# Kernel optimization log

Hardware: AMD Instinct MI355X
Metric: run time of the kernel (lower is better)

Reference implementation:

```python
import jax, jax.numpy as jnp
import numpy as np

CAPS = 16          # num_capsules
DIM = 16           # capsule_dim
NUM_ROUTING = 3
L2_EPS = 1e-12     # tf.nn.l2_normalize epsilon


def setup_inputs() -> dict:
    key = jax.random.key(0)
    k1, k2 = jax.random.split(key)
    inputs = jax.random.normal(k1, (16, 64, 64, 128), dtype=jnp.float32)
    # Conv2D kernel, HWIO layout, fan-in scaled like glorot-ish init
    kernel = jax.random.normal(k2, (3, 3, 128, CAPS * DIM), dtype=jnp.float32) * 0.03
    bias = jnp.zeros((CAPS * DIM,), dtype=jnp.float32)
    return {"inputs": inputs, "kernel": kernel, "bias": bias}


def reference(inputs, kernel, bias):
    # Conv2D(caps*dim, 3x3, padding='same', activation='relu'), channels_last
    x = jax.lax.conv_general_dilated(
        inputs, kernel, window_strides=(1, 1), padding="SAME",
        dimension_numbers=("NHWC", "HWIO", "NHWC"))
    x = jax.nn.relu(x + bias)
    B, H, W, _ = x.shape
    x = x.reshape(B, H * W, CAPS, DIM)            # (B, N, C, D)
    b = jnp.zeros((B, H * W, CAPS), dtype=x.dtype)
    v = None
    for _ in range(NUM_ROUTING):
        c = jax.nn.softmax(b, axis=-1)             # over capsules
        s = jnp.einsum("bnc,bncd->bcd", c, x)      # weighted sum over spatial
        # tf.nn.l2_normalize along last axis
        v = s * jax.lax.rsqrt(jnp.maximum(jnp.sum(s * s, axis=-1, keepdims=True), L2_EPS))
        b = b + jnp.einsum("bncd,bcd->bnc", x, v)  # agreement update
    # tile v over spatial dims: (B,1,1,C*D) -> (B,H,W,C*D)
    out = jnp.broadcast_to(v.reshape(B, 1, 1, CAPS * DIM), (B, H, W, CAPS * DIM))
    return out
```

## Files before the change

### kernel.cpp

```cpp
#include <hip/hip_runtime.h>
#include <hip/hip_bf16.h>

typedef unsigned short u16;
typedef unsigned int   u32;

typedef __bf16 bf16x8 __attribute__((ext_vector_type(8)));
typedef float  f32x4  __attribute__((ext_vector_type(4)));

__device__ __forceinline__ u16 f2b(float f) {
    __hip_bfloat16 h = __float2bfloat16(f);
    u16 u; __builtin_memcpy(&u, &h, 2); return u;
}
__device__ __forceinline__ float blo(u32 u) { return __uint_as_float(u << 16); }
__device__ __forceinline__ float bhi(u32 u) { return __uint_as_float(u & 0xffff0000u); }

__global__ void k_prep(const float* __restrict__ wk,
                       u16* __restrict__ BF, float* __restrict__ stats) {
    int bx = blockIdx.x, tid = threadIdx.x;
    if (bx < 1152) {
        int t = bx * 256 + tid;
        int j  = t & 7;
        int n  = (t >> 3) & 255;
        int q  = (t >> 11) & 3;
        int kk = (t >> 13) & 3;
        int p  = t >> 15;
        BF[t] = f2b(wk[(p * 128 + kk * 32 + q * 8 + j) * 256 + n]);
    } else {
        stats[(bx - 1152) * 256 + tid] = 0.f;
    }
}

__launch_bounds__(512, 4)
__global__ void k_conv(const float* __restrict__ in, const u16* __restrict__ BF,
                       const float* __restrict__ bias,
                       u16* __restrict__ X, float* __restrict__ s0) {
    __shared__ u16 ldsA[25344];
    const int t = threadIdx.x;
    const int lane = t & 63, wid = t >> 6;
    const int q = lane >> 4, l15 = lane & 15;
    const int wr = wid >> 2;
    const int wc = wid & 3;
    const int bb = blockIdx.x >> 6;
    const int h  = blockIdx.x & 63;
    const int wn0 = wc << 6;

#define STAGE_ALL() { \
    float4 fa[7], fb[7]; float zf[7]; \
    _Pragma("unroll") for (int i = 0; i < 7; ++i) { \
        int slot = i * 512 + t; \
        int ok = (i < 6) | (t < 96); \
        int pr = slot / 1056; int rem = slot - pr * 1056; \
        int wp = rem >> 4, cs = rem & 15; \
        int gc = cs ^ (wp & 7); \
        int y = h + pr - 1, x = wp - 1; \
        int inb = ok & ((((unsigned)y < 64u) & ((unsigned)x < 64u)) ? 1 : 0); \
        int ys = inb ? y : 0, xs = inb ? x : 0; \
        const float4* s4 = (const float4*)(in + \
            (((bb * 64 + ys) * 64 + xs) * 128 + gc * 8)); \
        fa[i] = s4[0]; fb[i] = s4[1]; \
        zf[i] = inb ? 1.f : 0.f; \
    } \
    _Pragma("unroll") for (int i = 0; i < 7; ++i) { \
        if (i < 6 || t < 96) { \
            int slot = i * 512 + t; \
            u16 ov[8]; \
            ov[0]=f2b(fa[i].x*zf[i]); ov[1]=f2b(fa[i].y*zf[i]); \
            ov[2]=f2b(fa[i].z*zf[i]); ov[3]=f2b(fa[i].w*zf[i]); \
            ov[4]=f2b(fb[i].x*zf[i]); ov[5]=f2b(fb[i].y*zf[i]); \
            ov[6]=f2b(fb[i].z*zf[i]); ov[7]=f2b(fb[i].w*zf[i]); \
            uint4 wv; __builtin_memcpy(&wv, ov, 16); \
            *(uint4*)((char*)ldsA + slot * 16) = wv; \
        } \
    } }

#define LOADB4(B, P, G) { \
    _Pragma("unroll") for (int ni = 0; ni < 4; ++ni) \
        B[ni] = *(const bf16x8*)(BFl + (P) * 32768 + (G) * 8192 + ni * 128); }

#define COMP4(B, DH, DW, G) { \
    bf16x8 af[2]; \
    _Pragma("unroll") for (int mi = 0; mi < 2; ++mi) { \
        int wp = wr * 32 + mi * 16 + l15 + (DW); \
        int swz = ((G) * 4 + q) ^ (wp & 7); \
        af[mi] = *(const bf16x8*)((const char*)ldsA + \
            (((DH) * 1056 + wp * 16 + swz) << 4)); \
    } \
    _Pragma("unroll") for (int mi = 0; mi < 2; ++mi) \
    _Pragma("unroll") for (int ni = 0; ni < 4; ++ni) \
        acc[mi][ni] = __builtin_amdgcn_mfma_f32_16x16x32_bf16( \
            af[mi], B[ni], acc[mi][ni], 0, 0, 0); }

#define CHAIN() { \
    LOADB4(B0, 0, 2); COMP4(B1, 0, 0, 1); \
    LOADB4(B1, 0, 3); COMP4(B0, 0, 0, 2); \
    LOADB4(B0, 1, 0); COMP4(B1, 0, 0, 3); \
    LOADB4(B1, 1, 1); COMP4(B0, 0, 1, 0); \
    LOADB4(B0, 1, 2); COMP4(B1, 0, 1, 1); \
    LOADB4(B1, 1, 3); COMP4(B0, 0, 1, 2); \
    LOADB4(B0, 2, 0); COMP4(B1, 0, 1, 3); \
    LOADB4(B1, 2, 1); COMP4(B0, 0, 2, 0); \
    LOADB4(B0, 2, 2); COMP4(B1, 0, 2, 1); \
    LOADB4(B1, 2, 3); COMP4(B0, 0, 2, 2); \
    LOADB4(B0, 3, 0); COMP4(B1, 0, 2, 3); \
    LOADB4(B1, 3, 1); COMP4(B0, 1, 0, 0); \
    LOADB4(B0, 3, 2); COMP4(B1, 1, 0, 1); \
    LOADB4(B1, 3, 3); COMP4(B0, 1, 0, 2); \
    LOADB4(B0, 4, 0); COMP4(B1, 1, 0, 3); \
    LOADB4(B1, 4, 1); COMP4(B0, 1, 1, 0); \
    LOADB4(B0, 4, 2); COMP4(B1, 1, 1, 1); \
    LOADB4(B1, 4, 3); COMP4(B0, 1, 1, 2); \
    LOADB4(B0, 5, 0); COMP4(B1, 1, 1, 3); \
    LOADB4(B1, 5, 1); COMP4(B0, 1, 2, 0); \
    LOADB4(B0, 5, 2); COMP4(B1, 1, 2, 1); \
    LOADB4(B1, 5, 3); COMP4(B0, 1, 2, 2); \
    LOADB4(B0, 6, 0); COMP4(B1, 1, 2, 3); \
    LOADB4(B1, 6, 1); COMP4(B0, 2, 0, 0); \
    LOADB4(B0, 6, 2); COMP4(B1, 2, 0, 1); \
    LOADB4(B1, 6, 3); COMP4(B0, 2, 0, 2); \
    LOADB4(B0, 7, 0); COMP4(B1, 2, 0, 3); \
    LOADB4(B1, 7, 1); COMP4(B0, 2, 1, 0); \
    LOADB4(B0, 7, 2); COMP4(B1, 2, 1, 1); \
    LOADB4(B1, 7, 3); COMP4(B0, 2, 1, 2); \
    LOADB4(B0, 8, 0); COMP4(B1, 2, 1, 3); \
    LOADB4(B1, 8, 1); COMP4(B0, 2, 2, 0); \
    LOADB4(B0, 8, 2); COMP4(B1, 2, 2, 1); \
    LOADB4(B1, 8, 3); COMP4(B0, 2, 2, 2); \
                      COMP4(B1, 2, 2, 3); }

    const u16* BFl = BF + (q * 2048 + (wn0 + l15) * 8);

    STAGE_ALL();

    f32x4 zero = {0.f, 0.f, 0.f, 0.f};
    f32x4 acc[2][4];
    #pragma unroll
    for (int mi = 0; mi < 2; ++mi)
        #pragma unroll
        for (int ni = 0; ni < 4; ++ni) acc[mi][ni] = zero;

    bf16x8 B0[4], B1[4];
    LOADB4(B0, 0, 0);
    LOADB4(B1, 0, 1);
    __syncthreads();

    COMP4(B0, 0, 0, 0);
    CHAIN();

    float bv[4];
    #pragma unroll
    for (int ni = 0; ni < 4; ++ni) bv[ni] = bias[wn0 + ni * 16 + l15];
    float colsum[4] = {0.f, 0.f, 0.f, 0.f};
    u16* xrow = X + (((bb << 12) + (h << 6) + wr * 32 + q * 4) * 256) + wn0 + l15;
    #pragma unroll
    for (int mi = 0; mi < 2; ++mi) {
        #pragma unroll
        for (int rr = 0; rr < 4; ++rr) {
            u16* xp = xrow + (mi * 16 + rr) * 256;
            #pragma unroll
            for (int ni = 0; ni < 4; ++ni) {
                float v = acc[mi][ni][rr] + bv[ni];
                v = v > 0.f ? v : 0.f;
                xp[ni * 16] = f2b(v);
                colsum[ni] += v;
            }
        }
    }
    #pragma unroll
    for (int ni = 0; ni < 4; ++ni) {
        float c = colsum[ni];
        c += __shfl_xor(c, 16);
        c += __shfl_xor(c, 32);
        if (lane < 16) atomicAdd(&s0[bb * 256 + wn0 + ni * 16 + l15], c);
    }
#undef STAGE_ALL
#undef LOADB4
#undef COMP4
#undef CHAIN
}

__launch_bounds__(256, 4)
__global__ void k_pass(const u16* __restrict__ X, const float* __restrict__ Sa,
                       const float* __restrict__ Sb, float* __restrict__ Sout,
                       int use2) {
    __shared__ float vs[272];
    __shared__ float red[4 * 272];
    const int t = threadIdx.x, b = blockIdx.y, chunk = blockIdx.x;
    const int c = t & 15, nl = t >> 4;
    const int lane = t & 63, wid = t >> 6;
    {
        float sa = Sa[b * 256 + t];
        float ss = sa * sa;
        #pragma unroll
        for (int off = 1; off < 16; off <<= 1) ss += __shfl_xor(ss, off);
        ss = ss < 1e-12f ? 1e-12f : ss;
        float vv = sa / sqrtf(ss);
        if (use2) {
            float sb = Sb[b * 256 + t];
            float s2v = sb * sb;
            #pragma unroll
            for (int off = 1; off < 16; off <<= 1) s2v += __shfl_xor(s2v, off);
            s2v = s2v < 1e-12f ? 1e-12f : s2v;
            vv += sb / sqrtf(s2v);
        }
        vs[(t >> 4) * 17 + (t & 15)] = vv;
    }
    const u16* xbase = X + ((b << 12) + chunk * 64 + nl) * 256 + c * 16;
    uint4 pa[8];
    #pragma unroll
    for (int r = 0; r < 4; ++r) {
        pa[2 * r]     = ((const uint4*)(xbase + r * 4096))[0];
        pa[2 * r + 1] = ((const uint4*)(xbase + r * 4096))[1];
    }
    __syncthreads();
    float vr[16];
    #pragma unroll
    for (int d = 0; d < 16; ++d) vr[d] = vs[c * 17 + d];

    float acc[16];
    #pragma unroll
    for (int d = 0; d < 16; ++d) acc[d] = 0.f;

    #pragma unroll
    for (int r = 0; r < 4; ++r) {
        u32 us[8];
        __builtin_memcpy(us, &pa[2 * r], 32);
        float xf[16];
        #pragma unroll
        for (int j = 0; j < 8; ++j) { xf[2*j] = blo(us[j]); xf[2*j+1] = bhi(us[j]); }
        float bvv = 0.f;
        #pragma unroll
        for (int d = 0; d < 16; ++d) bvv += xf[d] * vr[d];
        float e = __expf(bvv);
        float sm = e;
        #pragma unroll
        for (int off = 1; off < 16; off <<= 1) sm += __shfl_xor(sm, off);
        float w = e / sm;
        #pragma unroll
        for (int d = 0; d < 16; ++d) acc[d] += w * xf[d];
    }
    #pragma unroll
    for (int d = 0; d < 16; ++d) {
        acc[d] += __shfl_xor(acc[d], 16);
        acc[d] += __shfl_xor(acc[d], 32);
    }
    if (lane < 16) {
        #pragma unroll
        for (int d = 0; d < 16; ++d) red[wid * 272 + lane * 17 + d] = acc[d];
    }
    __syncthreads();
    {
        int c2 = t >> 4, d2 = t & 15;
        float tot = red[c2 * 17 + d2]       + red[272 + c2 * 17 + d2]
                  + red[544 + c2 * 17 + d2] + red[816 + c2 * 17 + d2];
        atomicAdd(&Sout[b * 256 + t], tot);
    }
}

__launch_bounds__(256, 4)
__global__ void k_bcast(const float* __restrict__ S, float* __restrict__ Out) {
    __shared__ float vls[256];
    int t = threadIdx.x, bx = blockIdx.x, b = blockIdx.y;
    float s = S[b * 256 + t];
    float ss = s * s;
    #pragma unroll
    for (int off = 1; off < 16; off <<= 1) ss += __shfl_xor(ss, off);
    ss = ss < 1e-12f ? 1e-12f : ss;
    vls[t] = s / sqrtf(ss);
    __syncthreads();
    float4 myv = ((const float4*)vls)[t & 63];
    float4* o = (float4*)Out + (long)b * 262144 + bx * 4096;
    #pragma unroll
    for (int j = 0; j < 16; ++j) o[j * 256 + t] = myv;
}

extern "C" void kernel_launch(void* const* d_in, const int* in_sizes, int n_in,
                              void* d_out, int out_size, void* d_ws, size_t ws_size,
                              hipStream_t stream) {
    const float* in   = (const float*)d_in[0];
    const float* wk   = (const float*)d_in[1];
    const float* bias = (const float*)d_in[2];
    float* out = (float*)d_out;
    char* ws = (char*)d_ws;

    const size_t OFF_BF  = 0;
    const size_t OFF_X   = 589824;
    const size_t OFF_ST  = 34144256;
    const size_t NEEDED  = OFF_ST + 3 * 16384;
    if (ws_size < NEEDED) return;

    u16* BF  = (u16*)(ws + OFF_BF);
    u16* X   = (u16*)(ws + OFF_X);
    float* s0 = (float*)(ws + OFF_ST);
    float* s2 = s0 + 4096;
    float* s3 = s2 + 4096;

    k_prep <<<1200, 256, 0, stream>>>(wk, BF, s0);
    k_conv <<<1024, 512, 0, stream>>>(in, BF, bias, X, s0);
    k_pass <<<dim3(64, 16), 256, 0, stream>>>(X, s0, s0, s2, 0);
    k_pass <<<dim3(64, 16), 256, 0, stream>>>(X, s0, s2, s3, 1);
    k_bcast<<<dim3(64, 16), 256, 0, stream>>>(s3, out);
}
```

Baseline: 166.8 us.

## Split conv LDS input tile into channel halves and double B prefetch depth

The conv kernel's shared-memory input tile is relaid out as two 64-channel halves, each with 8 swizzled 16-byte slots per pixel instead of 16. The weight prefetch now loads 8 fragments (two K-groups) per step, which halves the number of pipeline stages. The change aims to reduce LDS bank conflicts and issue overhead and to give more loads in flight per stage, at the cost of more VGPRs for the larger double-buffered B registers.

```diff
diff --git a/kernel.cpp b/kernel.cpp
--- a/kernel.cpp
+++ b/kernel.cpp
@@ -49,9 +49,10 @@
     _Pragma("unroll") for (int i = 0; i < 7; ++i) { \
         int slot = i * 512 + t; \
         int ok = (i < 6) | (t < 96); \
-        int pr = slot / 1056; int rem = slot - pr * 1056; \
-        int wp = rem >> 4, cs = rem & 15; \
-        int gc = cs ^ (wp & 7); \
+        int S = slot / 1584; int r2 = slot - S * 1584; \
+        int pr = r2 / 528; int rem = r2 - pr * 528; \
+        int wp = rem >> 3, cs = rem & 7; \
+        int gc = S * 8 + (cs ^ (wp & 7)); \
         int y = h + pr - 1, x = wp - 1; \
         int inb = ok & ((((unsigned)y < 64u) & ((unsigned)x < 64u)) ? 1 : 0); \
         int ys = inb ? y : 0, xs = inb ? x : 0; \
@@ -73,59 +74,25 @@
         } \
     } }
 
-#define LOADB4(B, P, G) { \
+#define LOADB8(B, P, S2) { \
+    _Pragma("unroll") for (int kk = 0; kk < 2; ++kk) \
     _Pragma("unroll") for (int ni = 0; ni < 4; ++ni) \
-        B[ni] = *(const bf16x8*)(BFl + (P) * 32768 + (G) * 8192 + ni * 128); }
-
-#define COMP4(B, DH, DW, G) { \
-    bf16x8 af[2]; \
-    _Pragma("unroll") for (int mi = 0; mi < 2; ++mi) { \
-        int wp = wr * 32 + mi * 16 + l15 + (DW); \
-        int swz = ((G) * 4 + q) ^ (wp & 7); \
-        af[mi] = *(const bf16x8*)((const char*)ldsA + \
-            (((DH) * 1056 + wp * 16 + swz) << 4)); \
-    } \
-    _Pragma("unroll") for (int mi = 0; mi < 2; ++mi) \
-    _Pragma("unroll") for (int ni = 0; ni < 4; ++ni) \
-        acc[mi][ni] = __builtin_amdgcn_mfma_f32_16x16x32_bf16( \
-            af[mi], B[ni], acc[mi][ni], 0, 0, 0); }
-
-#define CHAIN() { \
-    LOADB4(B0, 0, 2); COMP4(B1, 0, 0, 1); \
-    LOADB4(B1, 0, 3); COMP4(B0, 0, 0, 2); \
-    LOADB4(B0, 1, 0); COMP4(B1, 0, 0, 3); \
-    LOADB4(B1, 1, 1); COMP4(B0, 0, 1, 0); \
-    LOADB4(B0, 1, 2); COMP4(B1, 0, 1, 1); \
-    LOADB4(B1, 1, 3); COMP4(B0, 0, 1, 2); \
-    LOADB4(B0, 2, 0); COMP4(B1, 0, 1, 3); \
-    LOADB4(B1, 2, 1); COMP4(B0, 0, 2, 0); \
-    LOADB4(B0, 2, 2); COMP4(B1, 0, 2, 1); \
-    LOADB4(B1, 2, 3); COMP4(B0, 0, 2, 2); \
-    LOADB4(B0, 3, 0); COMP4(B1, 0, 2, 3); \
-    LOADB4(B1, 3, 1); COMP4(B0, 1, 0, 0); \
-    LOADB4(B0, 3, 2); COMP4(B1, 1, 0, 1); \
-    LOADB4(B1, 3, 3); COMP4(B0, 1, 0, 2); \
-    LOADB4(B0, 4, 0); COMP4(B1, 1, 0, 3); \
-    LOADB4(B1, 4, 1); COMP4(B0, 1, 1, 0); \
-    LOADB4(B0, 4, 2); COMP4(B1, 1, 1, 1); \
-    LOADB4(B1, 4, 3); COMP4(B0, 1, 1, 2); \
-    LOADB4(B0, 5, 0); COMP4(B1, 1, 1, 3); \
-    LOADB4(B1, 5, 1); COMP4(B0, 1, 2, 0); \
-    LOADB4(B0, 5, 2); COMP4(B1, 1, 2, 1); \
-    LOADB4(B1, 5, 3); COMP4(B0, 1, 2, 2); \
-    LOADB4(B0, 6, 0); COMP4(B1, 1, 2, 3); \
-    LOADB4(B1, 6, 1); COMP4(B0, 2, 0, 0); \
-    LOADB4(B0, 6, 2); COMP4(B1, 2, 0, 1); \
-    LOADB4(B1, 6, 3); COMP4(B0, 2, 0, 2); \
-    LOADB4(B0, 7, 0); COMP4(B1, 2, 0, 3); \
-    LOADB4(B1, 7, 1); COMP4(B0, 2, 1, 0); \
-    LOADB4(B0, 7, 2); COMP4(B1, 2, 1, 1); \
-    LOADB4(B1, 7, 3); COMP4(B0, 2, 1, 2); \
-    LOADB4(B0, 8, 0); COMP4(B1, 2, 1, 3); \
-    LOADB4(B1, 8, 1); COMP4(B0, 2, 2, 0); \
-    LOADB4(B0, 8, 2); COMP4(B1, 2, 2, 1); \
-    LOADB4(B1, 8, 3); COMP4(B0, 2, 2, 2); \
-                      COMP4(B1, 2, 2, 3); }
+        B[kk * 4 + ni] = *(const bf16x8*)(BFl + (P) * 32768 + \
+                                          ((S2) * 2 + kk) * 8192 + ni * 128); }
+
+#define COMP8(B, DH, DW, S2) { \
+    _Pragma("unroll") for (int kk = 0; kk < 2; ++kk) { \
+        bf16x8 af[2]; \
+        _Pragma("unroll") for (int mi = 0; mi < 2; ++mi) { \
+            int wp = wr * 32 + mi * 16 + l15 + (DW); \
+            int swz = (kk * 4 + q) ^ (wp & 7); \
+            af[mi] = *(const bf16x8*)((const char*)ldsA + \
+                (((S2) * 1584 + (DH) * 528 + wp * 8 + swz) << 4)); \
+        } \
+        _Pragma("unroll") for (int mi = 0; mi < 2; ++mi) \
+        _Pragma("unroll") for (int ni = 0; ni < 4; ++ni) \
+            acc[mi][ni] = __builtin_amdgcn_mfma_f32_16x16x32_bf16( \
+                af[mi], B[kk * 4 + ni], acc[mi][ni], 0, 0, 0); } }
 
     const u16* BFl = BF + (q * 2048 + (wn0 + l15) * 8);
 
@@ -138,13 +105,29 @@
         #pragma unroll
         for (int ni = 0; ni < 4; ++ni) acc[mi][ni] = zero;
 
-    bf16x8 B0[4], B1[4];
-    LOADB4(B0, 0, 0);
-    LOADB4(B1, 0, 1);
-    __syncthreads();
-
-    COMP4(B0, 0, 0, 0);
-    CHAIN();
+    bf16x8 B0[8], B1[8];
+    LOADB8(B0, 0, 0);
+    LOADB8(B1, 0, 1);
+    __syncthreads();
+
+    COMP8(B0, 0, 0, 0);
+    LOADB8(B0, 1, 0); COMP8(B1, 0, 0, 1);
+    LOADB8(B1, 1, 1); COMP8(B0, 0, 1, 0);
+    LOADB8(B0, 2, 0); COMP8(B1, 0, 1, 1);
+    LOADB8(B1, 2, 1); COMP8(B0, 0, 2, 0);
+    LOADB8(B0, 3, 0); COMP8(B1, 0, 2, 1);
+    LOADB8(B1, 3, 1); COMP8(B0, 1, 0, 0);
+    LOADB8(B0, 4, 0); COMP8(B1, 1, 0, 1);
+    LOADB8(B1, 4, 1); COMP8(B0, 1, 1, 0);
+    LOADB8(B0, 5, 0); COMP8(B1, 1, 1, 1);
+    LOADB8(B1, 5, 1); COMP8(B0, 1, 2, 0);
+    LOADB8(B0, 6, 0); COMP8(B1, 1, 2, 1);
+    LOADB8(B1, 6, 1); COMP8(B0, 2, 0, 0);
+    LOADB8(B0, 7, 0); COMP8(B1, 2, 0, 1);
+    LOADB8(B1, 7, 1); COMP8(B0, 2, 1, 0);
+    LOADB8(B0, 8, 0); COMP8(B1, 2, 1, 1);
+    LOADB8(B1, 8, 1); COMP8(B0, 2, 2, 0);
+                      COMP8(B1, 2, 2, 1);
 
     float bv[4];
     #pragma unroll
@@ -173,9 +156,8 @@
         if (lane < 16) atomicAdd(&s0[bb * 256 + wn0 + ni * 16 + l15], c);
     }
 #undef STAGE_ALL
-#undef LOADB4
-#undef COMP4
-#undef CHAIN
+#undef LOADB8
+#undef COMP8
 }
 
 __launch_bounds__(256, 4)
```

After: 166.0 us. No clear change (-0.5%).
